# Kernel optimization log

Measured on AMD Instinct MI355X. Metric: run time of the kernel, lower is better.

Reference implementation:

```python
import jax, jax.numpy as jnp
import numpy as np

I = 512   # input_size
H = 512   # hidden_size
NH = 2    # num_layers - 1 hidden cells
B = 8
S = 4096

def _unif(k, shape, fan_in):
    bound = 1.0 / np.sqrt(fan_in)
    return jax.random.uniform(k, shape, jnp.float32, -bound, bound)

def setup_inputs() -> dict:
    key = jax.random.key(0)
    ks = jax.random.split(key, 13)
    return {
        "xs": jax.random.normal(ks[0], (B, S, I), jnp.float32),
        # input cell
        "W_xh0": _unif(ks[1], (H, I), I), "b_xh0": _unif(ks[2], (H,), I),
        "W_hh0": _unif(ks[3], (H, H), H), "b_hh0": _unif(ks[4], (H,), H),
        "W_hy0": _unif(ks[5], (H, H), H), "b_hy0": _unif(ks[6], (H,), H),
        # hidden cells, stacked [NH, ...]
        "W_xh_h": _unif(ks[7], (NH, H, H), H), "b_xh_h": _unif(ks[8], (NH, H), H),
        "W_hh_h": _unif(ks[9], (NH, H, H), H), "b_hh_h": _unif(ks[10], (NH, H), H),
        "W_hy_h": _unif(ks[11], (NH, H, H), H), "b_hy_h": _unif(ks[12], (NH, H), H),
    }

def reference(xs, W_xh0, b_xh0, W_hh0, b_hh0, W_hy0, b_hy0,
              W_xh_h, b_xh_h, W_hh_h, b_hh_h, W_hy_h, b_hy_h):
    # NOTE: the original torch forward never passes hs back into the input
    # cell across timesteps (hs is re-zeroed each step), so timesteps are
    # fully independent and we process all (B*S) tokens at once.
    b, s, i = xs.shape
    x = xs.reshape(b * s, i)
    # input cell: hs=0 so W_hh contributes only its bias
    h = jnp.tanh(x @ W_xh0.T + b_xh0 + b_hh0)
    y = h @ W_hy0.T + b_hy0
    # hidden cells (dropout p=0.0 -> identity)
    for li in range(W_xh_h.shape[0]):
        h = jnp.tanh(h @ W_hh_h[li].T + b_hh_h[li] + y @ W_xh_h[li].T + b_xh_h[li])
        y = h @ W_hy_h[li].T + b_hy_h[li]
    outputs = y.reshape(b, s, -1).transpose(1, 0, 2)      # [S, B, H] like torch.stack
    hs_final = h.reshape(b, s, -1)[:, -1, :]              # last timestep, last layer
    return outputs, hs_final
```

## Files before the change

kernel.cpp:

```cpp
#include <hip/hip_runtime.h>
#include <hip/hip_fp16.h>

typedef _Float16 f16;
typedef f16 f16x4 __attribute__((ext_vector_type(4)));
typedef f16 f16x8 __attribute__((ext_vector_type(8)));
typedef float f32x4 __attribute__((ext_vector_type(4)));

#define NTOK 32768
#define KDIM 512
#define SLEN 4096
#define BATCH 8
#define WSZ  262144

__device__ __forceinline__ float fast_tanh(float x) {
    float ax = fabsf(x);
    float t = __expf(-2.0f * ax);
    float r = (1.0f - t) / (1.0f + t);
    return copysignf(r, x);
}

__device__ __forceinline__ void load_wf(f16x8 (&wf)[4], const f16* __restrict__ wp,
                                        int j0w, int fr, int col)
{
    #pragma unroll
    for (int jt = 0; jt < 4; ++jt)
        wf[jt] = *(const f16x8*)&wp[(size_t)(j0w + jt * 16 + fr) * KDIM + col];
}

__device__ __forceinline__ void half_mt(f32x4 (&acc)[4][8], const f16 (*hbuf)[512],
                                        const f16x8 (&wf)[4], int kt, int fr, int q, int mt0)
{
    f16x8 hf[4];
    #pragma unroll
    for (int i = 0; i < 4; ++i) {
        const int m = (mt0 + i) * 16 + fr;
        const int c = (kt * 4 + q) ^ (m & 7);
        hf[i] = *(const f16x8*)&hbuf[m][c << 3];
    }
    __builtin_amdgcn_s_setprio(1);
    #pragma unroll
    for (int jt = 0; jt < 4; ++jt)
        #pragma unroll
        for (int i = 0; i < 4; ++i)
            acc[jt][mt0 + i] = __builtin_amdgcn_mfma_f32_16x16x32_f16(
                wf[jt], hf[i], acc[jt][mt0 + i], 0, 0, 0);
    __builtin_amdgcn_s_setprio(0);
}

__device__ __forceinline__ void gemm_ktloop(f32x4 (&acc)[4][8], const f16 (*hbuf)[512],
                                            const f16* __restrict__ wp, f16x8 (&wfA)[4],
                                            int j0w, int fr, int q)
{
    f16x8 wfB[4];
    for (int kt = 0; kt < 16; kt += 2) {
        load_wf(wfB, wp, j0w, fr, (kt + 1) * 32 + q * 8);
        half_mt(acc, hbuf, wfA, kt, fr, q, 0);
        half_mt(acc, hbuf, wfA, kt, fr, q, 4);
        load_wf(wfA, wp, j0w, fr, (kt + 2) * 32 + q * 8);
        half_mt(acc, hbuf, wfB, kt + 1, fr, q, 0);
        half_mt(acc, hbuf, wfB, kt + 1, fr, q, 4);
    }
}

__global__ __launch_bounds__(512, 2)
void chain_kernel(const float* __restrict__ xs,
                  const f16*  __restrict__ Wp,
                  const float* __restrict__ bias,
                  float* __restrict__ out)
{
    __shared__ f16 hbuf[128][512];

    const int tid  = threadIdx.x;
    const int bid  = blockIdx.x;
    const int n0   = bid * 128;
    const int lane = tid & 63;
    const int wave = tid >> 6;
    const int fr   = lane & 15;
    const int q    = lane >> 4;
    const int j0w  = wave * 64;

    {
        const int tk = tid >> 2;
        const int cq = tid & 3;
        const float* __restrict__ src = &xs[(size_t)(n0 + tk) * KDIM];
        #pragma unroll
        for (int kt = 0; kt < 16; ++kt) {
            const int k = kt * 32 + cq * 8;
            const float4 v0 = *(const float4*)&src[k];
            const float4 v1 = *(const float4*)&src[k + 4];
            f16x8 h;
            h[0]=(f16)v0.x; h[1]=(f16)v0.y; h[2]=(f16)v0.z; h[3]=(f16)v0.w;
            h[4]=(f16)v1.x; h[5]=(f16)v1.y; h[6]=(f16)v1.z; h[7]=(f16)v1.w;
            const int c = (k >> 3) ^ (tk & 7);
            *(f16x8*)&hbuf[tk][c << 3] = h;
        }
    }

    f32x4 acc[4][8];

    for (int ph = 0; ph < 3; ++ph) {
        const f16*   __restrict__ wp = Wp + (size_t)ph * WSZ;
        const float* __restrict__ bp = bias + ph * KDIM;

        f16x8 wfA[4];
        load_wf(wfA, wp, j0w, fr, q * 8);

        f32x4 bv[4];
        #pragma unroll
        for (int jt = 0; jt < 4; ++jt)
            bv[jt] = *(const f32x4*)&bp[j0w + jt * 16 + q * 4];
        #pragma unroll
        for (int jt = 0; jt < 4; ++jt)
            #pragma unroll
            for (int mt = 0; mt < 8; ++mt)
                acc[jt][mt] = bv[jt];

        __syncthreads();

        gemm_ktloop(acc, hbuf, wp, wfA, j0w, fr, q);

        __syncthreads();

        #pragma unroll
        for (int jt = 0; jt < 4; ++jt) {
            const int j0f  = j0w + jt * 16 + q * 4;
            const int c    = j0f >> 3;
            const int half = j0f & 7;
            #pragma unroll
            for (int mt = 0; mt < 8; ++mt) {
                const int m = mt * 16 + fr;
                f16x4 hv;
                hv[0] = (f16)fast_tanh(acc[jt][mt][0]);
                hv[1] = (f16)fast_tanh(acc[jt][mt][1]);
                hv[2] = (f16)fast_tanh(acc[jt][mt][2]);
                hv[3] = (f16)fast_tanh(acc[jt][mt][3]);
                *(f16x4*)&hbuf[m][((c ^ (m & 7)) << 3) + half] = hv;
            }
        }
    }

    {
        const f16*   __restrict__ wp = Wp + (size_t)3 * WSZ;
        const float* __restrict__ bp = bias + 3 * KDIM;

        f16x8 wfA[4];
        load_wf(wfA, wp, j0w, fr, q * 8);

        f32x4 bv[4];
        #pragma unroll
        for (int jt = 0; jt < 4; ++jt)
            bv[jt] = *(const f32x4*)&bp[j0w + jt * 16 + q * 4];
        #pragma unroll
        for (int jt = 0; jt < 4; ++jt)
            #pragma unroll
            for (int mt = 0; mt < 8; ++mt)
                acc[jt][mt] = bv[jt];

        __syncthreads();

        if ((bid & 31) == 31) {
            const int f = tid;
            const int c = (f >> 3) ^ 7;
            out[(size_t)SLEN * BATCH * KDIM + (size_t)(bid >> 5) * KDIM + f] =
                (float)hbuf[127][(c << 3) + (f & 7)];
        }

        gemm_ktloop(acc, hbuf, wp, wfA, j0w, fr, q);

        #pragma unroll
        for (int jt = 0; jt < 4; ++jt) {
            const int j = j0w + jt * 16 + q * 4;
            #pragma unroll
            for (int mt = 0; mt < 8; ++mt) {
                const int n  = n0 + mt * 16 + fr;
                const int s  = n & (SLEN - 1);
                const int bb = n >> 12;
                *(f32x4*)&out[(size_t)(s * BATCH + bb) * KDIM + j] = acc[jt][mt];
            }
        }
    }
}

__device__ __forceinline__ void cvt2048(const float* __restrict__ src, f16* __restrict__ dst, int t)
{
    const float4 v0 = *(const float4*)&src[(size_t)t * 8];
    const float4 v1 = *(const float4*)&src[(size_t)t * 8 + 4];
    f16x8 h;
    h[0]=(f16)v0.x; h[1]=(f16)v0.y; h[2]=(f16)v0.z; h[3]=(f16)v0.w;
    h[4]=(f16)v1.x; h[5]=(f16)v1.y; h[6]=(f16)v1.z; h[7]=(f16)v1.w;
    *(f16x8*)&dst[(size_t)t * 8] = h;
}

__global__ __launch_bounds__(256)
void prep_mega(const float* __restrict__ W_xh0, const float* __restrict__ W_xh_h,
               const float* __restrict__ W_hh_h, const float* __restrict__ W_hy0,
               const float* __restrict__ W_hy_h,
               const float* __restrict__ b_xh0, const float* __restrict__ b_hh0,
               const float* __restrict__ b_xh_h, const float* __restrict__ b_hh_h,
               const float* __restrict__ b_hy0, const float* __restrict__ b_hy_h,
               f16* __restrict__ Wp, float* __restrict__ bias)
{
    __shared__ f16 A_s[128][64];
    __shared__ f16 B_s[128][64];

    const int b = blockIdx.x, tid = threadIdx.x;
    const int lane = tid & 63, wave = tid >> 6;

    if (b < 128) { cvt2048(W_xh0, Wp, b * 256 + tid); return; }
    if (b < 256) { cvt2048(W_hy_h + WSZ, Wp + 3 * WSZ, (b - 128) * 256 + tid); return; }

    if (b < 272) {
        const int bb = b - 256;
        const int li = bb >> 3;
        const int j0 = (bb & 7) * 64 + wave * 16;
        const float* __restrict__ W  = W_xh_h + (size_t)li * WSZ;
        const float* __restrict__ bh = li ? b_hy_h : b_hy0;
        const float4 h0 = *(const float4*)&bh[lane * 8];
        const float4 h1 = *(const float4*)&bh[lane * 8 + 4];
        for (int jj = 0; jj < 16; ++jj) {
            const int j = j0 + jj;
            const float4 w0 = *(const float4*)&W[(size_t)j * 512 + lane * 8];
            const float4 w1 = *(const float4*)&W[(size_t)j * 512 + lane * 8 + 4];
            float s = w0.x*h0.x + w0.y*h0.y + w0.z*h0.z + w0.w*h0.w
                    + w1.x*h1.x + w1.y*h1.y + w1.z*h1.z + w1.w*h1.w;
            #pragma unroll
            for (int off = 32; off; off >>= 1) s += __shfl_xor(s, off, 64);
            if (lane == 0)
                bias[(1 + li) * KDIM + j] =
                    b_hh_h[li * KDIM + j] + b_xh_h[li * KDIM + j] + s;
        }
        return;
    }

    if (b == 272) {
        #pragma unroll
        for (int u = 0; u < 2; ++u) {
            const int j = u * 256 + tid;
            bias[j] = b_xh0[j] + b_hh0[j];
            bias[3 * KDIM + j] = b_hy_h[KDIM + j];
        }
        return;
    }

    {
        const int fb   = b - 273;
        const int fold = fb >> 4;
        const int bid  = fb & 15;
        const float* __restrict__ A    = W_xh_h + (size_t)fold * WSZ;
        const float* __restrict__ Why  = fold ? W_hy_h : W_hy0;
        const float* __restrict__ Cadd = W_hh_h + (size_t)fold * WSZ;
        f16*         __restrict__ Cp   = Wp + WSZ + (size_t)fold * WSZ;

        const int n0 = (bid >> 2) * 128;
        const int j0 = (bid & 3) * 128;

        const int wm = wave >> 1, wn = wave & 1;
        const int fr = lane & 15, q = lane >> 4, sw = fr & 7;

        const int ar  = tid >> 1;
        const int ac0 = (tid & 1) * 4;
        const int bk  = tid >> 2;
        const int bjq = tid & 3;

        f32x4 acc[4][4] = {};

        for (int kt = 0; kt < 8; ++kt) {
            const int k0 = kt * 64;
            __syncthreads();
            #pragma unroll
            for (int cc = 0; cc < 4; ++cc) {
                const int c = ac0 + cc;
                const int k = k0 + c * 8;
                const float4 v0 = *(const float4*)&A[(size_t)(n0 + ar) * 512 + k];
                const float4 v1 = *(const float4*)&A[(size_t)(n0 + ar) * 512 + k + 4];
                f16x8 h;
                h[0]=(f16)v0.x; h[1]=(f16)v0.y; h[2]=(f16)v0.z; h[3]=(f16)v0.w;
                h[4]=(f16)v1.x; h[5]=(f16)v1.y; h[6]=(f16)v1.z; h[7]=(f16)v1.w;
                *(f16x8*)&A_s[ar][(c ^ (ar & 7)) << 3] = h;
            }
            {
                const int c  = bk >> 3;
                const int ke = bk & 7;
                #pragma unroll
                for (int u = 0; u < 8; ++u) {
                    const int jl = bjq * 32 + u * 4;
                    const float4 v = *(const float4*)&Why[(size_t)(k0 + bk) * 512 + j0 + jl];
                    B_s[jl + 0][(((c) ^ ((jl + 0) & 7)) << 3) + ke] = (f16)v.x;
                    B_s[jl + 1][(((c) ^ ((jl + 1) & 7)) << 3) + ke] = (f16)v.y;
                    B_s[jl + 2][(((c) ^ ((jl + 2) & 7)) << 3) + ke] = (f16)v.z;
                    B_s[jl + 3][(((c) ^ ((jl + 3) & 7)) << 3) + ke] = (f16)v.w;
                }
            }
            __syncthreads();
            #pragma unroll
            for (int kc = 0; kc < 8; kc += 4) {
                f16x8 a[4], bfr[4];
                #pragma unroll
                for (int t = 0; t < 4; ++t)
                    a[t] = *(const f16x8*)&A_s[wm * 64 + t * 16 + fr][((kc + q) ^ sw) << 3];
                #pragma unroll
                for (int t = 0; t < 4; ++t)
                    bfr[t] = *(const f16x8*)&B_s[wn * 64 + t * 16 + fr][((kc + q) ^ sw) << 3];
                #pragma unroll
                for (int im = 0; im < 4; ++im)
                    #pragma unroll
                    for (int jn = 0; jn < 4; ++jn)
                        acc[im][jn] = __builtin_amdgcn_mfma_f32_16x16x32_f16(
                            a[im], bfr[jn], acc[im][jn], 0, 0, 0);
            }
        }

        const int r0 = q * 4, c = fr;
        #pragma unroll
        for (int jn = 0; jn < 4; ++jn) {
            const int j = j0 + wn * 64 + jn * 16 + c;
            #pragma unroll
            for (int im = 0; im < 4; ++im)
                #pragma unroll
                for (int r = 0; r < 4; ++r) {
                    const int n = n0 + wm * 64 + im * 16 + r0 + r;
                    Cp[(size_t)n * KDIM + j] =
                        (f16)(acc[im][jn][r] + Cadd[(size_t)n * KDIM + j]);
                }
        }
    }
}

extern "C" void kernel_launch(void* const* d_in, const int* in_sizes, int n_in,
                              void* d_out, int out_size, void* d_ws, size_t ws_size,
                              hipStream_t stream)
{
    (void)in_sizes; (void)n_in; (void)out_size; (void)ws_size;

    const float* xs     = (const float*)d_in[0];
    const float* W_xh0  = (const float*)d_in[1];
    const float* b_xh0  = (const float*)d_in[2];
    const float* b_hh0  = (const float*)d_in[4];
    const float* W_hy0  = (const float*)d_in[5];
    const float* b_hy0  = (const float*)d_in[6];
    const float* W_xh_h = (const float*)d_in[7];
    const float* b_xh_h = (const float*)d_in[8];
    const float* W_hh_h = (const float*)d_in[9];
    const float* b_hh_h = (const float*)d_in[10];
    const float* W_hy_h = (const float*)d_in[11];
    const float* b_hy_h = (const float*)d_in[12];

    f16*   Wp   = (f16*)d_ws;
    float* bias = (float*)(Wp + 4 * WSZ);

    prep_mega<<<305, dim3(256), 0, stream>>>(W_xh0, W_xh_h, W_hh_h, W_hy0, W_hy_h,
                                             b_xh0, b_hh0, b_xh_h, b_hh_h,
                                             b_hy0, b_hy_h, Wp, bias);
    chain_kernel<<<256, dim3(512), 0, stream>>>(xs, Wp, bias, (float*)d_out);
}
```

Baseline: 251.7 us.

## Software-pipeline LDS fragment loads ahead of MFMAs and use rcp in tanh

Splits the LDS fragment load from the MFMA block so that the next group of h fragments is loaded into a second register set while the current MFMAs run. The k-loop is now fully unrolled and its indices wrap with a mask. This is meant to hide LDS latency behind matrix work. tanh also uses a hardware reciprocal in place of a divide. The cost is higher register pressure under launch_bounds(512,2), and the wrapped indices issue a few redundant loads on the last iteration.

```diff
diff --git a/kernel.cpp b/kernel.cpp
--- a/kernel.cpp
+++ b/kernel.cpp
@@ -15,7 +15,7 @@
 __device__ __forceinline__ float fast_tanh(float x) {
     float ax = fabsf(x);
     float t = __expf(-2.0f * ax);
-    float r = (1.0f - t) / (1.0f + t);
+    float r = (1.0f - t) * __builtin_amdgcn_rcpf(1.0f + t);
     return copysignf(r, x);
 }
 
@@ -27,16 +27,20 @@
         wf[jt] = *(const f16x8*)&wp[(size_t)(j0w + jt * 16 + fr) * KDIM + col];
 }
 
-__device__ __forceinline__ void half_mt(f32x4 (&acc)[4][8], const f16 (*hbuf)[512],
-                                        const f16x8 (&wf)[4], int kt, int fr, int q, int mt0)
-{
-    f16x8 hf[4];
+__device__ __forceinline__ void load_hf4(f16x8 (&hf)[4], const f16 (*hbuf)[512],
+                                         int kt, int fr, int q, int mt0)
+{
     #pragma unroll
     for (int i = 0; i < 4; ++i) {
         const int m = (mt0 + i) * 16 + fr;
         const int c = (kt * 4 + q) ^ (m & 7);
         hf[i] = *(const f16x8*)&hbuf[m][c << 3];
     }
+}
+
+__device__ __forceinline__ void mfma16(f32x4 (&acc)[4][8], const f16x8 (&wf)[4],
+                                       const f16x8 (&hf)[4], int mt0)
+{
     __builtin_amdgcn_s_setprio(1);
     #pragma unroll
     for (int jt = 0; jt < 4; ++jt)
@@ -51,14 +55,20 @@
                                             const f16* __restrict__ wp, f16x8 (&wfA)[4],
                                             int j0w, int fr, int q)
 {
-    f16x8 wfB[4];
+    f16x8 wfB[4], hfP[4], hfQ[4];
+    load_hf4(hfP, hbuf, 0, fr, q, 0);
+    #pragma unroll
     for (int kt = 0; kt < 16; kt += 2) {
-        load_wf(wfB, wp, j0w, fr, (kt + 1) * 32 + q * 8);
-        half_mt(acc, hbuf, wfA, kt, fr, q, 0);
-        half_mt(acc, hbuf, wfA, kt, fr, q, 4);
-        load_wf(wfA, wp, j0w, fr, (kt + 2) * 32 + q * 8);
-        half_mt(acc, hbuf, wfB, kt + 1, fr, q, 0);
-        half_mt(acc, hbuf, wfB, kt + 1, fr, q, 4);
+        load_wf(wfB, wp, j0w, fr, ((kt + 1) & 15) * 32 + q * 8);
+        load_hf4(hfQ, hbuf, kt, fr, q, 4);
+        mfma16(acc, wfA, hfP, 0);
+        load_hf4(hfP, hbuf, (kt + 1) & 15, fr, q, 0);
+        mfma16(acc, wfA, hfQ, 4);
+        load_wf(wfA, wp, j0w, fr, ((kt + 2) & 15) * 32 + q * 8);
+        load_hf4(hfQ, hbuf, (kt + 1) & 15, fr, q, 4);
+        mfma16(acc, wfB, hfP, 0);
+        load_hf4(hfP, hbuf, (kt + 2) & 15, fr, q, 0);
+        mfma16(acc, wfB, hfQ, 4);
     }
 }
 
```

Result: slower. 284.6 us (+13.1%).
